# Kernel tuning notes

Hardware: AMD Instinct MI355X
Metric: run time of the kernel (lower is better)

The kernel has to match this reference:

```python
import jax, jax.numpy as jnp
import numpy as np

B, K, VOC, D = 1024, 5, 32000, 128


def setup_inputs() -> dict:
    key = jax.random.key(0)
    k1, k2, k3, k4, k5 = jax.random.split(key, 5)
    return {
        "vi": jax.random.normal(k1, (B, VOC), dtype=jnp.float32),
        "vo": jax.random.normal(k2, (B, VOC), dtype=jnp.float32),
        "neg_samples": jax.random.normal(k3, (B, K, VOC), dtype=jnp.float32),
        "V": jax.random.normal(k4, (VOC, D), dtype=jnp.float32),
        "U": jax.random.normal(k5, (VOC, D), dtype=jnp.float32),
    }


def reference(vi, vo, neg_samples, V, U):
    # one-hot-style matmul embedding lookups
    vi_embed = vi @ V                                  # [B, D]
    vo_embed = vo @ U                                  # [B, D]
    # positive term: logsigmoid(<vi_embed, vo_embed>)
    left = jax.nn.log_sigmoid(jnp.sum(vi_embed * vo_embed, axis=1, keepdims=True))  # [B, 1]
    # negative samples: [B, K, D] then batched dot with vi_embed
    neg_embed = jnp.einsum("bkv,vd->bkd", neg_samples, U)   # [B, K, D]
    batch_mul = jnp.einsum("bkd,bd->bk", neg_embed, vi_embed)  # [B, K]
    right = jnp.sum(jax.nn.log_sigmoid(-batch_mul), axis=1, keepdims=True)  # [B, 1]
    return jnp.mean(-(left + right))
```

## Files before the change

### kernel.cpp

```cpp
#include <hip/hip_runtime.h>
#include <hip/hip_bf16.h>

#define B_SZ 1024
#define KNEG 5
#define VOC 32000
#define DIM 128

typedef __bf16 bf16x8 __attribute__((ext_vector_type(8)));
typedef float f32x4 __attribute__((ext_vector_type(4)));


__device__ __forceinline__ float logsig(float x) {
    return fminf(x, 0.0f) - log1pf(expf(-fabsf(x)));
}

__global__ __launch_bounds__(256) void k0_convert(
    const float* __restrict__ V, const float* __restrict__ U,
    __bf16* __restrict__ Vt, __bf16* __restrict__ Ub) {
    __shared__ float tile[32][33];
    int bid = blockIdx.x;
    int vt = bid >> 2;
    int dt = bid & 3;
    int v0 = vt * 32, d0 = dt * 32;
    int t = threadIdx.x;
    int lr = t >> 5;
    int lc = t & 31;
#pragma unroll
    for (int i = 0; i < 4; ++i) {
        int r = lr + i * 8;
        size_t idx = (size_t)(v0 + r) * DIM + d0 + lc;
        tile[r][lc] = V[idx];
        Ub[idx] = (__bf16)U[idx];
    }
    __syncthreads();
#pragma unroll
    for (int i = 0; i < 4; ++i) {
        int r = lr + i * 8;
        Vt[(size_t)(d0 + r) * VOC + v0 + lc] = (__bf16)tile[lc][r];
    }
}

__global__ __launch_bounds__(256) void k1_viembed(
    const float* __restrict__ vi, const __bf16* __restrict__ Vt,
    float* __restrict__ partial) {
    int mt = blockIdx.x;
    int sp = blockIdx.y;
    int wave = threadIdx.x >> 6;
    int lane = threadIdx.x & 63;
    int n16 = lane & 15;
    int q = lane >> 4;
    int b0 = mt * 32;

    f32x4 acc[2][8];
#pragma unroll
    for (int rt = 0; rt < 2; ++rt)
#pragma unroll
        for (int ct = 0; ct < 8; ++ct)
            acc[rt][ct] = (f32x4){0.f, 0.f, 0.f, 0.f};

    int v_base = sp * 4000;
    for (int s = wave; s < 125; s += 4) {
        int kk = v_base + s * 32 + q * 8;
        bf16x8 afrag[2];
#pragma unroll
        for (int rt = 0; rt < 2; ++rt) {
            int b = b0 + rt * 16 + n16;
            const float4* p = (const float4*)(vi + (size_t)b * VOC + kk);
            float4 x0 = p[0];
            float4 x1 = p[1];
            bf16x8 a;
            a[0] = (__bf16)x0.x; a[1] = (__bf16)x0.y;
            a[2] = (__bf16)x0.z; a[3] = (__bf16)x0.w;
            a[4] = (__bf16)x1.x; a[5] = (__bf16)x1.y;
            a[6] = (__bf16)x1.z; a[7] = (__bf16)x1.w;
            afrag[rt] = a;
        }
#pragma unroll
        for (int ct = 0; ct < 8; ++ct) {
            int d = ct * 16 + n16;
            bf16x8 bfrag = *(const bf16x8*)(Vt + (size_t)d * VOC + kk);
#pragma unroll
            for (int rt = 0; rt < 2; ++rt)
                acc[rt][ct] = __builtin_amdgcn_mfma_f32_16x16x32_bf16(
                    afrag[rt], bfrag, acc[rt][ct], 0, 0, 0);
        }
    }

    __shared__ float red[4][32][128];
#pragma unroll
    for (int rt = 0; rt < 2; ++rt)
#pragma unroll
        for (int ct = 0; ct < 8; ++ct)
#pragma unroll
            for (int r = 0; r < 4; ++r)
                red[wave][rt * 16 + q * 4 + r][ct * 16 + n16] = acc[rt][ct][r];
    __syncthreads();
    int t = threadIdx.x;
#pragma unroll
    for (int i = 0; i < 16; ++i) {
        int idx = t + i * 256;
        int bl = idx >> 7, dd = idx & 127;
        float s = red[0][bl][dd] + red[1][bl][dd] + red[2][bl][dd] + red[3][bl][dd];
        partial[((size_t)sp * B_SZ + b0 + bl) * DIM + dd] = s;
    }
}

__global__ __launch_bounds__(256) void k2_reduce(
    const float* __restrict__ partial, __bf16* __restrict__ vie) {
    int idx = blockIdx.x * 256 + threadIdx.x;
    float s = 0.f;
#pragma unroll
    for (int sp = 0; sp < 8; ++sp) s += partial[(size_t)sp * (B_SZ * DIM) + idx];
    vie[idx] = (__bf16)s;
}

__global__ __launch_bounds__(256) void k3_fused(
    const __bf16* __restrict__ vie, const float* __restrict__ vo,
    const float* __restrict__ neg, const __bf16* __restrict__ Ub,
    float* __restrict__ pos_dot, float* __restrict__ neg_dot) {
    int bt = blockIdx.x;
    int vc = blockIdx.y;
    int wave = threadIdx.x >> 6;
    int lane = threadIdx.x & 63;
    int n16 = lane & 15;
    int q = lane >> 4;
    int b0 = bt * 32;

    bf16x8 afrag[2][4];
#pragma unroll
    for (int rt = 0; rt < 2; ++rt) {
        int b = b0 + rt * 16 + n16;
#pragma unroll
        for (int ks = 0; ks < 4; ++ks)
            afrag[rt][ks] = *(const bf16x8*)(vie + (size_t)b * DIM + ks * 32 + q * 8);
    }

    float posA[2][4];
    float negA[2][4][KNEG];
#pragma unroll
    for (int rt = 0; rt < 2; ++rt)
#pragma unroll
        for (int r = 0; r < 4; ++r) {
            posA[rt][r] = 0.f;
#pragma unroll
            for (int k = 0; k < KNEG; ++k) negA[rt][r][k] = 0.f;
        }

    int vbase = vc * 1280;
    for (int tv = wave; tv < 80; tv += 4) {
        int v0 = vbase + tv * 16;
        f32x4 w0 = (f32x4){0.f, 0.f, 0.f, 0.f};
        f32x4 w1 = (f32x4){0.f, 0.f, 0.f, 0.f};
#pragma unroll
        for (int ks = 0; ks < 4; ++ks) {
            bf16x8 bfrag = *(const bf16x8*)(Ub + (size_t)(v0 + n16) * DIM + ks * 32 + q * 8);
            w0 = __builtin_amdgcn_mfma_f32_16x16x32_bf16(afrag[0][ks], bfrag, w0, 0, 0, 0);
            w1 = __builtin_amdgcn_mfma_f32_16x16x32_bf16(afrag[1][ks], bfrag, w1, 0, 0, 0);
        }
        int v = v0 + n16;
#pragma unroll
        for (int rt = 0; rt < 2; ++rt) {
#pragma unroll
            for (int r = 0; r < 4; ++r) {
                int b = b0 + rt * 16 + q * 4 + r;
                float wv = (rt == 0) ? w0[r] : w1[r];
                posA[rt][r] += vo[(size_t)b * VOC + v] * wv;
                const float* np_ = neg + ((size_t)b * KNEG) * VOC + v;
#pragma unroll
                for (int k = 0; k < KNEG; ++k)
                    negA[rt][r][k] += np_[(size_t)k * VOC] * wv;
            }
        }
    }

#pragma unroll
    for (int rt = 0; rt < 2; ++rt)
#pragma unroll
        for (int r = 0; r < 4; ++r) {
            int b = b0 + rt * 16 + q * 4 + r;
            float p = posA[rt][r];
            p += __shfl_xor(p, 1, 16);
            p += __shfl_xor(p, 2, 16);
            p += __shfl_xor(p, 4, 16);
            p += __shfl_xor(p, 8, 16);
            if (n16 == 0) atomicAdd(&pos_dot[b], p);
#pragma unroll
            for (int k = 0; k < KNEG; ++k) {
                float nv = negA[rt][r][k];
                nv += __shfl_xor(nv, 1, 16);
                nv += __shfl_xor(nv, 2, 16);
                nv += __shfl_xor(nv, 4, 16);
                nv += __shfl_xor(nv, 8, 16);
                if (n16 == 0) atomicAdd(&neg_dot[b * KNEG + k], nv);
            }
        }
}

__global__ __launch_bounds__(256) void k4_final(
    const float* __restrict__ pos_dot, const float* __restrict__ neg_dot,
    float* __restrict__ out) {
    __shared__ float wsum[4];
    int t = threadIdx.x;
    float s = 0.f;
    for (int b = t; b < B_SZ; b += 256) {
        float left = logsig(pos_dot[b]);
        float right = 0.f;
#pragma unroll
        for (int k = 0; k < KNEG; ++k) right += logsig(-neg_dot[b * KNEG + k]);
        s += -(left + right);
    }
#pragma unroll
    for (int m = 32; m >= 1; m >>= 1) s += __shfl_xor(s, m, 64);
    if ((t & 63) == 0) wsum[t >> 6] = s;
    __syncthreads();
    if (t == 0) out[0] = (wsum[0] + wsum[1] + wsum[2] + wsum[3]) * (1.0f / B_SZ);
}

extern "C" void kernel_launch(void* const* d_in, const int* in_sizes, int n_in,
                              void* d_out, int out_size, void* d_ws, size_t ws_size,
                              hipStream_t stream) {
    const float* vi  = (const float*)d_in[0];
    const float* vo  = (const float*)d_in[1];
    const float* neg = (const float*)d_in[2];
    const float* V   = (const float*)d_in[3];
    const float* U   = (const float*)d_in[4];

    char* ws = (char*)d_ws;
    __bf16* Ub      = (__bf16*)(ws);
    __bf16* Vt      = (__bf16*)(ws + 8192000);
    float*  partial = (float*) (ws + 16384000);
    __bf16* vie     = (__bf16*)(ws + 20578304);
    float*  pos_dot = (float*) (ws + 20840448);
    float*  neg_dot = (float*) (ws + 20844544);
    float*  out     = (float*)d_out;

    hipMemsetAsync(ws + 20840448, 0, 4096 + 20480, stream);

    k0_convert<<<4000, 256, 0, stream>>>(V, U, Vt, Ub);
    k1_viembed<<<dim3(32, 8), 256, 0, stream>>>(vi, Vt, partial);
    k2_reduce<<<512, 256, 0, stream>>>(partial, vie);
    k3_fused<<<dim3(32, 25), 256, 0, stream>>>(vie, vo, neg, Ub, pos_dot, neg_dot);
    k4_final<<<1, 256, 0, stream>>>(pos_dot, neg_dot, out);
}
```

Before: 1.128 ms.

## Stage MFMA results in LDS so vo/neg streams are read with coalesced float4 loads

```diff
diff --git a/kernel.cpp b/kernel.cpp
--- a/kernel.cpp
+++ b/kernel.cpp
@@ -118,12 +118,11 @@
     const __bf16* __restrict__ vie, const float* __restrict__ vo,
     const float* __restrict__ neg, const __bf16* __restrict__ Ub,
     float* __restrict__ pos_dot, float* __restrict__ neg_dot) {
+    __shared__ float W[32 * 256];
     int bt = blockIdx.x;
     int vc = blockIdx.y;
-    int wave = threadIdx.x >> 6;
-    int lane = threadIdx.x & 63;
-    int n16 = lane & 15;
-    int q = lane >> 4;
+    int t = threadIdx.x;
+    int wave = t >> 6, lane = t & 63, n16 = lane & 15, q = lane >> 4;
     int b0 = bt * 32;
 
     bf16x8 afrag[2][4];
@@ -135,65 +134,66 @@
             afrag[rt][ks] = *(const bf16x8*)(vie + (size_t)b * DIM + ks * 32 + q * 8);
     }
 
-    float posA[2][4];
-    float negA[2][4][KNEG];
-#pragma unroll
-    for (int rt = 0; rt < 2; ++rt)
-#pragma unroll
-        for (int r = 0; r < 4; ++r) {
-            posA[rt][r] = 0.f;
-#pragma unroll
-            for (int k = 0; k < KNEG; ++k) negA[rt][r][k] = 0.f;
-        }
+    int rowB = t >> 3;
+    int lcol = t & 7;
+    float acc[6] = {0.f, 0.f, 0.f, 0.f, 0.f, 0.f};
 
     int vbase = vc * 1280;
-    for (int tv = wave; tv < 80; tv += 4) {
-        int v0 = vbase + tv * 16;
-        f32x4 w0 = (f32x4){0.f, 0.f, 0.f, 0.f};
-        f32x4 w1 = (f32x4){0.f, 0.f, 0.f, 0.f};
-#pragma unroll
-        for (int ks = 0; ks < 4; ++ks) {
-            bf16x8 bfrag = *(const bf16x8*)(Ub + (size_t)(v0 + n16) * DIM + ks * 32 + q * 8);
-            w0 = __builtin_amdgcn_mfma_f32_16x16x32_bf16(afrag[0][ks], bfrag, w0, 0, 0, 0);
-            w1 = __builtin_amdgcn_mfma_f32_16x16x32_bf16(afrag[1][ks], bfrag, w1, 0, 0, 0);
-        }
-        int v = v0 + n16;
-#pragma unroll
-        for (int rt = 0; rt < 2; ++rt) {
+    const float* vop = vo + (size_t)(b0 + rowB) * VOC + vbase + lcol * 4;
+    const float* negp[KNEG];
+#pragma unroll
+    for (int k = 0; k < KNEG; ++k)
+        negp[k] = neg + ((size_t)(b0 + rowB) * KNEG + k) * VOC + vbase + lcol * 4;
+
+    for (int c = 0; c < 5; ++c) {
+        int vchunk = vbase + c * 256;
+#pragma unroll
+        for (int j = 0; j < 4; ++j) {
+            int tt = wave * 4 + j;
+            int v0 = vchunk + tt * 16;
+            f32x4 w0 = (f32x4){0.f, 0.f, 0.f, 0.f};
+            f32x4 w1 = (f32x4){0.f, 0.f, 0.f, 0.f};
+#pragma unroll
+            for (int ks = 0; ks < 4; ++ks) {
+                bf16x8 bfrag = *(const bf16x8*)(Ub + (size_t)(v0 + n16) * DIM + ks * 32 + q * 8);
+                w0 = __builtin_amdgcn_mfma_f32_16x16x32_bf16(afrag[0][ks], bfrag, w0, 0, 0, 0);
+                w1 = __builtin_amdgcn_mfma_f32_16x16x32_bf16(afrag[1][ks], bfrag, w1, 0, 0, 0);
+            }
+            int col = tt * 16 + n16;
 #pragma unroll
             for (int r = 0; r < 4; ++r) {
-                int b = b0 + rt * 16 + q * 4 + r;
-                float wv = (rt == 0) ? w0[r] : w1[r];
-                posA[rt][r] += vo[(size_t)b * VOC + v] * wv;
-                const float* np_ = neg + ((size_t)b * KNEG) * VOC + v;
-#pragma unroll
-                for (int k = 0; k < KNEG; ++k)
-                    negA[rt][r][k] += np_[(size_t)k * VOC] * wv;
+                W[(q * 4 + r) * 256 + col] = w0[r];
+                W[(16 + q * 4 + r) * 256 + col] = w1[r];
             }
         }
-    }
-
-#pragma unroll
-    for (int rt = 0; rt < 2; ++rt)
-#pragma unroll
-        for (int r = 0; r < 4; ++r) {
-            int b = b0 + rt * 16 + q * 4 + r;
-            float p = posA[rt][r];
-            p += __shfl_xor(p, 1, 16);
-            p += __shfl_xor(p, 2, 16);
-            p += __shfl_xor(p, 4, 16);
-            p += __shfl_xor(p, 8, 16);
-            if (n16 == 0) atomicAdd(&pos_dot[b], p);
+        __syncthreads();
+        const float* vpc = vop + c * 256;
+#pragma unroll
+        for (int i = 0; i < 8; ++i) {
+            float4 wv = *(const float4*)&W[rowB * 256 + lcol * 4 + i * 32];
+            float4 x = *(const float4*)(vpc + i * 32);
+            acc[0] += x.x * wv.x + x.y * wv.y + x.z * wv.z + x.w * wv.w;
 #pragma unroll
             for (int k = 0; k < KNEG; ++k) {
-                float nv = negA[rt][r][k];
-                nv += __shfl_xor(nv, 1, 16);
-                nv += __shfl_xor(nv, 2, 16);
-                nv += __shfl_xor(nv, 4, 16);
-                nv += __shfl_xor(nv, 8, 16);
-                if (n16 == 0) atomicAdd(&neg_dot[b * KNEG + k], nv);
+                float4 y = *(const float4*)(negp[k] + c * 256 + i * 32);
+                acc[1 + k] += y.x * wv.x + y.y * wv.y + y.z * wv.z + y.w * wv.w;
             }
         }
+        __syncthreads();
+    }
+
+#pragma unroll
+    for (int j = 0; j < 6; ++j) {
+        float s = acc[j];
+        s += __shfl_xor(s, 1, 8);
+        s += __shfl_xor(s, 2, 8);
+        s += __shfl_xor(s, 4, 8);
+        if (lcol == 0) {
+            int b = b0 + rowB;
+            if (j == 0) atomicAdd(&pos_dot[b], s);
+            else atomicAdd(&neg_dot[b * KNEG + (j - 1)], s);
+        }
+    }
 }
 
 __global__ __launch_bounds__(256) void k4_final(
```

Measured after the change: 1.120 ms. About the same (-0.7%).
